# Optimization experiments

Measured on AMD Instinct MI355X. Metric: run time of the kernel, lower is better.

The kernel has to match this reference:

```python
import jax, jax.numpy as jnp
import numpy as np

DIM = 512
HEADS = 8
DIM_HEAD = 64
HIDDEN = HEADS * DIM_HEAD  # 512
B, C, H, W = 32, DIM, 32, 32


def setup_inputs() -> dict:
    key = jax.random.key(0)
    ks = jax.random.split(key, 7)
    s_in = 1.0 / np.sqrt(DIM)
    s_h = 1.0 / np.sqrt(HIDDEN)
    x = jax.random.normal(ks[0], (B, C, H, W), dtype=jnp.float32)
    Wq = jax.random.uniform(ks[1], (DIM, HIDDEN), jnp.float32, -s_in, s_in)
    Wk = jax.random.uniform(ks[2], (DIM, HIDDEN), jnp.float32, -s_in, s_in)
    Wv = jax.random.uniform(ks[3], (DIM, HIDDEN), jnp.float32, -s_in, s_in)
    Wp = jax.random.uniform(ks[4], (HIDDEN, DIM), jnp.float32, -s_h, s_h)
    bp = jax.random.uniform(ks[5], (DIM,), jnp.float32, -s_h, s_h)
    return {"x": x, "Wq": Wq, "Wk": Wk, "Wv": Wv, "Wp": Wp, "bp": bp}


def reference(x, Wq, Wk, Wv, Wp, bp):
    b, c, h, w = x.shape
    n = h * w
    xt = x.reshape(b, c, n).transpose(0, 2, 1)  # [B, N, C]
    q = (xt @ Wq).reshape(b, n, HEADS, DIM_HEAD)
    k = (xt @ Wk).reshape(b, n, HEADS, DIM_HEAD)
    v = (xt @ Wv).reshape(b, n, HEADS, DIM_HEAD)
    k_softmax = jax.nn.softmax(k, axis=1)  # softmax over tokens N
    context = jnp.einsum('bnhd,bnhv->bhdv', k_softmax, v)  # [B, H, D, D]
    out = jnp.einsum('bnhd,bhdv->bnhv', q, context).reshape(b, n, HIDDEN)
    out = out @ Wp + bp  # [B, N, C]
    return out.transpose(0, 2, 1).reshape(b, c, h, w)
```

## Files before the change

kernel.cpp:

```cpp
#include <hip/hip_runtime.h>
#include <hip/hip_bf16.h>


__device__ __forceinline__ float bf2f(unsigned short u) {
    union { unsigned int i; float f; } x;
    x.i = ((unsigned int)u) << 16;
    return x.f;
}
__device__ __forceinline__ unsigned short f2bf(float f) {
    unsigned int u = __float_as_uint(f);
    unsigned int lsb = (u >> 16) & 1u;
    u += 0x7fffu + lsb;
    return (unsigned short)(u >> 16);
}

__device__ __forceinline__ void glds16(const unsigned short* g, unsigned short* l) {
    __builtin_amdgcn_global_load_lds(
        (const __attribute__((address_space(1))) unsigned int*)g,
        (__attribute__((address_space(3))) unsigned int*)l,
        16, 0, 0);
}

typedef __bf16 bf16x8 __attribute__((ext_vector_type(8)));
typedef float  f32x4  __attribute__((ext_vector_type(4)));

__global__ void detect_dtype(const unsigned short* __restrict__ x, int* __restrict__ flag)
{
    int t = threadIdx.x;
    unsigned short u = x[2 * t];
    int e = (u >> 7) & 0xFF;
    int sane = (e >= 113 && e <= 142) ? 1 : 0;
    #pragma unroll
    for (int off = 32; off > 0; off >>= 1) sane += __shfl_xor(sane, off, 64);
    if (t == 0) *flag = (sane >= 32) ? 1 : 0;
}

__global__ __launch_bounds__(256) void transpose_x(
    const void* __restrict__ in, unsigned short* __restrict__ out,
    const int* __restrict__ flag)
{
    const int fl = *flag;
    const int b  = blockIdx.z;
    const int c0 = blockIdx.x * 64;
    const int r0 = blockIdx.y * 64;
    __shared__ unsigned short Ts[64][68];
    const int t   = threadIdx.x;
    const int tr  = t >> 4;
    const int tc4 = (t & 15) * 4;
    #pragma unroll
    for (int rr = 0; rr < 4; ++rr) {
        int rl = rr * 16 + tr;
        long off = (long)b * 524288 + (long)(r0 + rl) * 1024 + c0 + tc4;
        unsigned short v[4];
        if (fl) {
            ushort4 u = *(const ushort4*)((const unsigned short*)in + off);
            v[0] = u.x; v[1] = u.y; v[2] = u.z; v[3] = u.w;
        } else {
            float4 u = *(const float4*)((const float*)in + off);
            v[0] = f2bf(u.x); v[1] = f2bf(u.y); v[2] = f2bf(u.z); v[3] = f2bf(u.w);
        }
        #pragma unroll
        for (int q = 0; q < 4; ++q) Ts[tc4 + q][rl] = v[q];
    }
    __syncthreads();
    #pragma unroll
    for (int rr = 0; rr < 4; ++rr) {
        int cl = rr * 16 + tr;
        ushort4 o = *(const ushort4*)&Ts[cl][tc4];
        *(ushort4*)(out + (long)b * 524288 + (long)(c0 + cl) * 512 + r0 + tc4) = o;
    }
}

__global__ __launch_bounds__(256) void transpose_w3(
    const void* __restrict__ w0, const void* __restrict__ w1,
    const void* __restrict__ w2, unsigned short* __restrict__ out,
    unsigned short* __restrict__ wqb,
    const int* __restrict__ flag)
{
    const int fl = *flag;
    const int z  = blockIdx.z;
    const void* in = (z == 0) ? w0 : (z == 1) ? w1 : w2;
    unsigned short* op = out + (long)z * 262144;
    const int c0 = blockIdx.x * 64;
    const int r0 = blockIdx.y * 64;
    __shared__ unsigned short Ts[64][68];
    const int t   = threadIdx.x;
    const int tr  = t >> 4;
    const int tc4 = (t & 15) * 4;
    #pragma unroll
    for (int rr = 0; rr < 4; ++rr) {
        int rl = rr * 16 + tr;
        long off = (long)(r0 + rl) * 512 + c0 + tc4;
        unsigned short v[4];
        if (fl) {
            ushort4 u = *(const ushort4*)((const unsigned short*)in + off);
            v[0] = u.x; v[1] = u.y; v[2] = u.z; v[3] = u.w;
        } else {
            float4 u = *(const float4*)((const float*)in + off);
            v[0] = f2bf(u.x); v[1] = f2bf(u.y); v[2] = f2bf(u.z); v[3] = f2bf(u.w);
        }
        if (z == 0) {
            ushort4 s; s.x = v[0]; s.y = v[1]; s.z = v[2]; s.w = v[3];
            *(ushort4*)(wqb + off) = s;
        }
        #pragma unroll
        for (int q = 0; q < 4; ++q) Ts[tc4 + q][rl] = v[q];
    }
    __syncthreads();
    #pragma unroll
    for (int rr = 0; rr < 4; ++rr) {
        int cl = rr * 16 + tr;
        ushort4 o = *(const ushort4*)&Ts[cl][tc4];
        *(ushort4*)(op + (long)(c0 + cl) * 512 + r0 + tc4) = o;
    }
}

__global__ __launch_bounds__(256) void gemm_bt_mfma(
    const unsigned short* __restrict__ A, long a_bstride,
    const unsigned short* __restrict__ Bm, long b_bstride,
    void* __restrict__ C, long c_bstride,
    const void* __restrict__ bias,
    int M, int N, int K, int mode,
    const int* __restrict__ flag)
{
    const int b  = blockIdx.z;
    const int n0 = blockIdx.x * 128;
    const int m0 = blockIdx.y * 128;
    const unsigned short* Ab = A  + (long)b * a_bstride;
    const unsigned short* Bb = Bm + (long)b * b_bstride;

    __shared__ unsigned short As[2 * 128 * 32];
    __shared__ unsigned short Bs[2 * 128 * 32];

    const int t    = threadIdx.x;
    const int w    = t >> 6;
    const int lane = t & 63;
    const int wm   = (w & 1) * 64;
    const int wn   = (w >> 1) * 64;
    const int fm   = lane & 15;
    const int kg   = lane >> 4;

    const int crow = lane >> 2;
    const int ccol = (lane & 3) * 8;

    f32x4 acc[4][4] = {};

    #pragma unroll
    for (int j = 0; j < 2; ++j) {
        const int chunk = w * 2 + j;
        const int row   = chunk * 16 + crow;
        glds16(Ab + (long)(m0 + row) * K + ccol, &As[chunk * 512]);
        glds16(Bb + (long)(n0 + row) * K + ccol, &Bs[chunk * 512]);
    }

    int cur = 0;
    for (int k0 = 0; k0 < K; k0 += 32) {
        __syncthreads();

        if (k0 + 32 < K) {
            const int kn  = k0 + 32;
            const int nxt = (cur ^ 1) * 4096;
            #pragma unroll
            for (int j = 0; j < 2; ++j) {
                const int chunk = w * 2 + j;
                const int row   = chunk * 16 + crow;
                glds16(Ab + (long)(m0 + row) * K + kn + ccol, &As[nxt + chunk * 512]);
                glds16(Bb + (long)(n0 + row) * K + kn + ccol, &Bs[nxt + chunk * 512]);
            }
        }

        const int bufo = cur * 4096;
        bf16x8 af[4], bf[4];
        #pragma unroll
        for (int i = 0; i < 4; ++i)
            af[i] = *(const bf16x8*)&As[bufo + (wm + i * 16 + fm) * 32 + kg * 8];
        #pragma unroll
        for (int j = 0; j < 4; ++j)
            bf[j] = *(const bf16x8*)&Bs[bufo + (wn + j * 16 + fm) * 32 + kg * 8];
        #pragma unroll
        for (int i = 0; i < 4; ++i)
            #pragma unroll
            for (int j = 0; j < 4; ++j)
                acc[i][j] = __builtin_amdgcn_mfma_f32_16x16x32_bf16(
                    bf[j], af[i], acc[i][j], 0, 0, 0);
        cur ^= 1;
    }

    const int fl = *flag;
    const long cb = (long)b * c_bstride;
    #pragma unroll
    for (int i = 0; i < 4; ++i) {
        const int m = m0 + wm + i * 16 + fm;
        float bv = 0.f;
        if (mode == 2 && bias)
            bv = fl ? bf2f(((const unsigned short*)bias)[m])
                    : ((const float*)bias)[m];
        #pragma unroll
        for (int j = 0; j < 4; ++j) {
            const int nb = n0 + wn + j * 16 + kg * 4;
            const long off = cb + (long)m * N + nb;
            if (mode == 0) {
                ushort4 o;
                o.x = f2bf(acc[i][j][0]); o.y = f2bf(acc[i][j][1]);
                o.z = f2bf(acc[i][j][2]); o.w = f2bf(acc[i][j][3]);
                *(ushort4*)&((unsigned short*)C)[off] = o;
            } else if (fl) {
                ushort4 o;
                o.x = f2bf(acc[i][j][0] + bv); o.y = f2bf(acc[i][j][1] + bv);
                o.z = f2bf(acc[i][j][2] + bv); o.w = f2bf(acc[i][j][3] + bv);
                *(ushort4*)&((unsigned short*)C)[off] = o;
            } else {
                float4 o;
                o.x = acc[i][j][0] + bv; o.y = acc[i][j][1] + bv;
                o.z = acc[i][j][2] + bv; o.w = acc[i][j][3] + bv;
                *(float4*)&((float*)C)[off] = o;
            }
        }
    }
}

__global__ __launch_bounds__(256) void ctx_softmax_mfma(
    const unsigned short* __restrict__ KV, float* __restrict__ ctx)
{
    const int bh = blockIdx.x;
    const unsigned short* Kb = KV + ((long)(bh >> 3) << 20) + (long)(bh & 7) * 65536;
    const unsigned short* Vb = Kb + 524288;

    const int t    = threadIdx.x;
    const int w    = t >> 6;
    const int lane = t & 63;
    const int fm   = lane & 15;
    const int kg   = lane >> 4;

    __shared__ float sm_m[64];
    __shared__ float sm_inv[64];

    {
        const int r = t >> 2;
        const int q = t & 3;
        const uint4* row = (const uint4*)(Kb + r * 1024 + q * 256);
        float mx = -3.402823466e+38f;
        #pragma unroll 8
        for (int i = 0; i < 32; ++i) {
            uint4 u = row[i];
            #pragma unroll
            for (int z = 0; z < 4; ++z) {
                unsigned int uu = ((const unsigned int*)&u)[z];
                float lo = bf2f((unsigned short)(uu & 0xffffu));
                float hi = bf2f((unsigned short)(uu >> 16));
                mx = fmaxf(mx, fmaxf(lo, hi));
            }
        }
        mx = fmaxf(mx, __shfl_xor(mx, 1, 64));
        mx = fmaxf(mx, __shfl_xor(mx, 2, 64));
        float s = 0.f;
        #pragma unroll 8
        for (int i = 0; i < 32; ++i) {
            uint4 u = row[i];
            #pragma unroll
            for (int z = 0; z < 4; ++z) {
                unsigned int uu = ((const unsigned int*)&u)[z];
                s += __expf(bf2f((unsigned short)(uu & 0xffffu)) - mx);
                s += __expf(bf2f((unsigned short)(uu >> 16)) - mx);
            }
        }
        s += __shfl_xor(s, 1, 64);
        s += __shfl_xor(s, 2, 64);
        if (q == 0) { sm_m[r] = mx; sm_inv[r] = 1.0f / s; }
    }
    __syncthreads();

    float rm[4], ri[4];
    #pragma unroll
    for (int i = 0; i < 4; ++i) {
        rm[i] = sm_m[i * 16 + fm];
        ri[i] = sm_inv[i * 16 + fm];
    }

    f32x4 acc[4][4] = {};

    #pragma unroll 2
    for (int c = 0; c < 8; ++c) {
        const int k0 = w * 256 + c * 32;
        bf16x8 af[4], bf[4];
        #pragma unroll
        for (int i = 0; i < 4; ++i) {
            uint4 u = *(const uint4*)(Kb + (long)(i * 16 + fm) * 1024 + k0 + kg * 8);
            unsigned short o[8];
            #pragma unroll
            for (int z = 0; z < 4; ++z) {
                unsigned int uu = ((const unsigned int*)&u)[z];
                float lo = __expf(bf2f((unsigned short)(uu & 0xffffu)) - rm[i]) * ri[i];
                float hi = __expf(bf2f((unsigned short)(uu >> 16))     - rm[i]) * ri[i];
                o[2 * z]     = f2bf(lo);
                o[2 * z + 1] = f2bf(hi);
            }
            af[i] = *(const bf16x8*)o;
        }
        #pragma unroll
        for (int j = 0; j < 4; ++j)
            bf[j] = *(const bf16x8*)(Vb + (long)(j * 16 + fm) * 1024 + k0 + kg * 8);
        #pragma unroll
        for (int i = 0; i < 4; ++i)
            #pragma unroll
            for (int j = 0; j < 4; ++j)
                acc[i][j] = __builtin_amdgcn_mfma_f32_16x16x32_bf16(
                    af[i], bf[j], acc[i][j], 0, 0, 0);
    }

    __shared__ float red[64][65];
    for (int ph = 0; ph < 4; ++ph) {
        if (w == ph) {
            #pragma unroll
            for (int i = 0; i < 4; ++i)
                #pragma unroll
                for (int j = 0; j < 4; ++j)
                    #pragma unroll
                    for (int r = 0; r < 4; ++r) {
                        const int m = i * 16 + kg * 4 + r;
                        const int n = j * 16 + fm;
                        if (ph == 0) red[m][n]  = acc[i][j][r];
                        else         red[m][n] += acc[i][j][r];
                    }
        }
        __syncthreads();
    }
    float* cp = ctx + (long)bh * 4096;
    for (int i = t; i < 4096; i += 256) cp[i] = red[i >> 6][i & 63];
}

__global__ __launch_bounds__(256) void weff_kernel(
    const float* __restrict__ ctx,
    const void* __restrict__ Wp,
    unsigned short* __restrict__ WeffT,
    const int* __restrict__ flag)
{
    const int fl = *flag;
    const int c0 = blockIdx.x * 64;
    const int h  = blockIdx.y;
    const int b  = blockIdx.z;

    __shared__ float Cs[64][65];
    __shared__ float Ws[64][68];

    const int t = threadIdx.x;
    const int tx = t & 15, ty = t >> 4;

    const float* cb = ctx + ((long)b * 8 + h) * 4096;
    for (int i = t; i < 4096; i += 256) Cs[i >> 6][i & 63] = cb[i];
    for (int i = t; i < 4096; i += 256) {
        int v = i >> 6, c = i & 63;
        long idx = (long)(h * 64 + v) * 512 + c0 + c;
        Ws[v][c] = fl ? bf2f(((const unsigned short*)Wp)[idx])
                      : ((const float*)Wp)[idx];
    }
    __syncthreads();

    float acc[4][4];
    #pragma unroll
    for (int i = 0; i < 4; ++i)
        #pragma unroll
        for (int j = 0; j < 4; ++j) acc[i][j] = 0.f;

    #pragma unroll
    for (int v = 0; v < 64; ++v) {
        float a[4], d[4];
        #pragma unroll
        for (int i = 0; i < 4; ++i) a[i] = Ws[v][ty * 4 + i];
        #pragma unroll
        for (int j = 0; j < 4; ++j) d[j] = Cs[tx * 4 + j][v];
        #pragma unroll
        for (int i = 0; i < 4; ++i)
            #pragma unroll
            for (int j = 0; j < 4; ++j) acc[i][j] += a[i] * d[j];
    }
    #pragma unroll
    for (int i = 0; i < 4; ++i) {
        ushort4 o;
        o.x = f2bf(acc[i][0]); o.y = f2bf(acc[i][1]);
        o.z = f2bf(acc[i][2]); o.w = f2bf(acc[i][3]);
        *(ushort4*)&WeffT[((long)b * 512 + c0 + ty * 4 + i) * 512 + h * 64 + tx * 4] = o;
    }
}

extern "C" void kernel_launch(void* const* d_in, const int* in_sizes, int n_in,
                              void* d_out, int out_size, void* d_ws, size_t ws_size,
                              hipStream_t stream) {
    const void* x  = d_in[0];
    const void* Wq = d_in[1];
    const void* Wk = d_in[2];
    const void* Wv = d_in[3];
    const void* Wp = d_in[4];
    const void* bp = d_in[5];

    char* ws = (char*)d_ws;
    unsigned short* Xt    = (unsigned short*)(ws);
    unsigned short* KV    = (unsigned short*)(ws + 33554432ll);
    unsigned short* Ft    = (unsigned short*)(ws + 33554432ll);
    float*          ctx   = (float*)(ws + 100663296ll);
    unsigned short* WeffT = (unsigned short*)(ws + 104857600ll);
    unsigned short* WT    = (unsigned short*)(ws + 121634816ll);
    unsigned short* Wqb   = (unsigned short*)(ws + 123207680ll);
    int*            flag  = (int*)(ws + 123731968ll);

    detect_dtype<<<dim3(1), dim3(64), 0, stream>>>((const unsigned short*)x, flag);

    transpose_x<<<dim3(16, 8, 32), 256, 0, stream>>>(x, Xt, flag);
    transpose_w3<<<dim3(8, 8, 3), 256, 0, stream>>>(Wq, Wk, Wv, WT, Wqb, flag);

    const long XB = 1024ll * 512;
    gemm_bt_mfma<<<dim3(8, 8, 32), 256, 0, stream>>>(
        WT + 262144, 0, Xt, XB, KV, 1048576ll, nullptr, 1024, 1024, 512, 0, flag);

    ctx_softmax_mfma<<<dim3(256), 256, 0, stream>>>(KV, ctx);

    weff_kernel<<<dim3(8, 8, 32), 256, 0, stream>>>(ctx, Wp, WeffT, flag);

    gemm_bt_mfma<<<dim3(4, 4, 32), 256, 0, stream>>>(
        WeffT, 262144ll, Wqb, 0, Ft, 262144ll, nullptr, 512, 512, 512, 0, flag);

    gemm_bt_mfma<<<dim3(8, 4, 32), 256, 0, stream>>>(
        Ft, 262144ll, Xt, XB, d_out, 524288ll, bp, 512, 1024, 512, 2, flag);
}
```

Baseline: 316.4 us.

## Add 256x256-tile MFMA GEMM with 512 threads for the K/V and output projections

```diff
diff --git a/kernel.cpp b/kernel.cpp
--- a/kernel.cpp
+++ b/kernel.cpp
@@ -112,6 +112,139 @@
         int cl = rr * 16 + tr;
         ushort4 o = *(const ushort4*)&Ts[cl][tc4];
         *(ushort4*)(op + (long)(c0 + cl) * 512 + r0 + tc4) = o;
+    }
+}
+
+__global__ __launch_bounds__(512, 2) void gemm_bt_256(
+    const unsigned short* __restrict__ A, long a_bstride,
+    const unsigned short* __restrict__ Bm, long b_bstride,
+    void* __restrict__ C, long c_bstride,
+    const void* __restrict__ bias,
+    int M, int N, int K, int mode,
+    const int* __restrict__ flag)
+{
+    const int b  = blockIdx.z;
+    const int n0 = blockIdx.x * 256;
+    const int m0 = blockIdx.y * 256;
+    const unsigned short* Ab = A  + (long)b * a_bstride;
+    const unsigned short* Bb = Bm + (long)b * b_bstride;
+
+    __shared__ unsigned short S[65536];
+
+    const int t  = threadIdx.x;
+    const int w  = t >> 6;
+    const int l  = t & 63;
+    const int fm = l & 15;
+    const int kg = l >> 4;
+    const int wr = w >> 2;
+    const int wc = w & 3;
+
+    const int rowb = w * 8 + (l >> 3);
+    const int swz  = ((l & 7) ^ (l >> 3)) * 8;
+    const unsigned short* gA = Ab + (long)(m0 + rowb) * K + swz;
+    const unsigned short* gB = Bb + (long)(n0 + rowb) * K + swz;
+
+    const int sA = fm & 7;
+
+    f32x4 acc[8][4] = {};
+
+    const int NT = K >> 6;
+
+    auto STAGE = [&](int kt, int buf) {
+        const long ko = (long)kt * 64;
+        unsigned short* Ld = &S[buf * 32768];
+        #pragma unroll
+        for (int r = 0; r < 4; ++r)
+            glds16(gA + (long)r * 64 * K + ko, Ld + r * 4096 + w * 512);
+        #pragma unroll
+        for (int r = 0; r < 4; ++r)
+            glds16(gB + (long)r * 64 * K + ko, Ld + 16384 + r * 4096 + w * 512);
+    };
+
+    STAGE(0, 0);
+
+    for (int tt = 0; tt < NT; ++tt) {
+        if (tt + 1 < NT) {
+            STAGE(tt + 1, (tt + 1) & 1);
+            __builtin_amdgcn_sched_barrier(0);
+            asm volatile("s_waitcnt vmcnt(8)" ::: "memory");
+        } else {
+            __builtin_amdgcn_sched_barrier(0);
+            asm volatile("s_waitcnt vmcnt(0)" ::: "memory");
+        }
+        __builtin_amdgcn_sched_barrier(0);
+        __builtin_amdgcn_s_barrier();
+        __builtin_amdgcn_sched_barrier(0);
+
+        {
+            const unsigned short* Abuf = &S[(tt & 1) * 32768];
+            const unsigned short* Bbuf = Abuf + 16384;
+            bf16x8 bf[4][2];
+            #pragma unroll
+            for (int j = 0; j < 4; ++j)
+                #pragma unroll
+                for (int kk = 0; kk < 2; ++kk) {
+                    const int row = wc * 64 + j * 16 + fm;
+                    bf[j][kk] = *(const bf16x8*)&Bbuf[row * 64 + ((kk * 4 + kg) ^ sA) * 8];
+                }
+            #pragma unroll
+            for (int q = 0; q < 4; ++q) {
+                bf16x8 af[2][2];
+                #pragma unroll
+                for (int ii = 0; ii < 2; ++ii)
+                    #pragma unroll
+                    for (int kk = 0; kk < 2; ++kk) {
+                        const int row = wr * 128 + (q * 2 + ii) * 16 + fm;
+                        af[ii][kk] = *(const bf16x8*)&Abuf[row * 64 + ((kk * 4 + kg) ^ sA) * 8];
+                    }
+                __builtin_amdgcn_s_setprio(1);
+                #pragma unroll
+                for (int ii = 0; ii < 2; ++ii)
+                    #pragma unroll
+                    for (int j = 0; j < 4; ++j)
+                        #pragma unroll
+                        for (int kk = 0; kk < 2; ++kk)
+                            acc[q * 2 + ii][j] = __builtin_amdgcn_mfma_f32_16x16x32_bf16(
+                                bf[j][kk], af[ii][kk], acc[q * 2 + ii][j], 0, 0, 0);
+                __builtin_amdgcn_s_setprio(0);
+            }
+        }
+
+        __builtin_amdgcn_sched_barrier(0);
+        __builtin_amdgcn_s_barrier();
+        __builtin_amdgcn_sched_barrier(0);
+    }
+
+    const int fl = *flag;
+    const long cb = (long)b * c_bstride;
+    #pragma unroll
+    for (int i = 0; i < 8; ++i) {
+        const int m = m0 + wr * 128 + i * 16 + fm;
+        float bv = 0.f;
+        if (mode == 2 && bias)
+            bv = fl ? bf2f(((const unsigned short*)bias)[m])
+                    : ((const float*)bias)[m];
+        #pragma unroll
+        for (int j = 0; j < 4; ++j) {
+            const int nb = n0 + wc * 64 + j * 16 + kg * 4;
+            const long off = cb + (long)m * N + nb;
+            if (mode == 0) {
+                ushort4 o;
+                o.x = f2bf(acc[i][j][0]); o.y = f2bf(acc[i][j][1]);
+                o.z = f2bf(acc[i][j][2]); o.w = f2bf(acc[i][j][3]);
+                *(ushort4*)&((unsigned short*)C)[off] = o;
+            } else if (fl) {
+                ushort4 o;
+                o.x = f2bf(acc[i][j][0] + bv); o.y = f2bf(acc[i][j][1] + bv);
+                o.z = f2bf(acc[i][j][2] + bv); o.w = f2bf(acc[i][j][3] + bv);
+                *(ushort4*)&((unsigned short*)C)[off] = o;
+            } else {
+                float4 o;
+                o.x = acc[i][j][0] + bv; o.y = acc[i][j][1] + bv;
+                o.z = acc[i][j][2] + bv; o.w = acc[i][j][3] + bv;
+                *(float4*)&((float*)C)[off] = o;
+            }
+        }
     }
 }
 
@@ -409,7 +542,7 @@
     transpose_w3<<<dim3(8, 8, 3), 256, 0, stream>>>(Wq, Wk, Wv, WT, Wqb, flag);
 
     const long XB = 1024ll * 512;
-    gemm_bt_mfma<<<dim3(8, 8, 32), 256, 0, stream>>>(
+    gemm_bt_256<<<dim3(4, 4, 32), 512, 0, stream>>>(
         WT + 262144, 0, Xt, XB, KV, 1048576ll, nullptr, 1024, 1024, 512, 0, flag);
 
     ctx_softmax_mfma<<<dim3(256), 256, 0, stream>>>(KV, ctx);
@@ -419,6 +552,6 @@
     gemm_bt_mfma<<<dim3(4, 4, 32), 256, 0, stream>>>(
         WeffT, 262144ll, Wqb, 0, Ft, 262144ll, nullptr, 512, 512, 512, 0, flag);
 
-    gemm_bt_mfma<<<dim3(8, 4, 32), 256, 0, stream>>>(
+    gemm_bt_256<<<dim3(4, 2, 32), 512, 0, stream>>>(
         Ft, 262144ll, Xt, XB, d_out, 524288ll, bp, 512, 1024, 512, 2, flag);
 }
```

Result: faster. 300.1 us (-5.2%).
